# Performance work log

Hardware: AMD Instinct MI355X
Metric: run time of the kernel (lower is better)

## Reference

```python
import jax, jax.numpy as jnp
import numpy as np


def setup_inputs() -> dict:
    key = jax.random.key(0)
    k1, k2 = jax.random.split(key)
    enc_output = jax.random.normal(k1, (4, 4096, 1024), dtype=jnp.float32)
    dec_output = jax.random.normal(k2, (4, 4096, 1024), dtype=jnp.float32)
    return {"enc_output": enc_output, "dec_output": dec_output}


def reference(enc_output, dec_output):
    # a_t[b, e, t] = sum_d enc[b, e, d] * dec[b, t, d]   -> [B, T_enc, T_dec]
    a_t = jnp.einsum('bed,btd->bet', enc_output, dec_output)
    # softmax over dim=1 (the T_enc axis), no scaling, no mask (faithful to source)
    a_t = jax.nn.softmax(a_t, axis=1)
    # c_t[b, t, d] = sum_e a_t[b, e, t] * enc[b, e, d]   -> [B, T_dec, D]
    c_t = jnp.einsum('bet,bed->btd', a_t, enc_output)
    return c_t
```

## Files before the change

kernel.cpp:

```cpp
#include <hip/hip_runtime.h>
#include <hip/hip_fp16.h>

typedef _Float16 half_t;
typedef _Float16 f16x8 __attribute__((ext_vector_type(8)));
typedef _Float16 f16x4 __attribute__((ext_vector_type(4)));
typedef float f32x4 __attribute__((ext_vector_type(4)));

#define SEQ 4096
#define DDIM 1024
#define NBATCH 4

__device__ __forceinline__ void gload16(const half_t* g, half_t* l) {
  __builtin_amdgcn_global_load_lds((const __attribute__((address_space(1))) void*)g,
                                   (__attribute__((address_space(3))) void*)l, 16, 0, 0);
}

__global__ __launch_bounds__(256) void conv_f16(const float* __restrict__ src,
                                                half_t* __restrict__ dst) {
  int i = blockIdx.x * 256 + threadIdx.x;
  float4 x = ((const float4*)src)[i];
  f16x4 o = {(half_t)x.x, (half_t)x.y, (half_t)x.z, (half_t)x.w};
  *(f16x4*)(dst + (size_t)i * 4) = o;
}

__global__ __launch_bounds__(256) void transpose_f16(const float* __restrict__ src,
                                                     half_t* __restrict__ dst) {
  __shared__ float tile[32][33];
  int b = blockIdx.z;
  int e0 = blockIdx.x * 32, d0 = blockIdx.y * 32;
  const float* s = src + (size_t)b * SEQ * DDIM;
  half_t* dt = dst + (size_t)b * DDIM * SEQ;
  int tx = threadIdx.x & 31, ty = threadIdx.x >> 5;
#pragma unroll
  for (int i = 0; i < 4; i++) {
    int e = e0 + ty + i * 8;
    tile[ty + i * 8][tx] = s[(size_t)e * DDIM + d0 + tx];
  }
  __syncthreads();
#pragma unroll
  for (int i = 0; i < 4; i++) {
    int d = d0 + ty + i * 8;
    dt[(size_t)d * SEQ + e0 + tx] = (half_t)tile[tx][ty + i * 8];
  }
}

#define BM 128
#define BN 128
#define BK 64

__global__ __launch_bounds__(256) void gemm_f16(const half_t* __restrict__ A,
                                                const half_t* __restrict__ B,
                                                float* __restrict__ C, int M, int N, int K) {
  __shared__ __align__(16) half_t As[BM * BK];
  __shared__ __align__(16) half_t Bs[BN * BK];
  const int tid = threadIdx.x;
  const int bm = blockIdx.x, bn = blockIdx.y;
  const int wave = tid >> 6, lane = tid & 63;
  const int wm = (wave & 1) * 64, wn = (wave >> 1) * 64;
  const int mrow = lane & 15, quad = lane >> 4;

  f32x4 acc[4][4];
#pragma unroll
  for (int i = 0; i < 4; i++)
#pragma unroll
    for (int j = 0; j < 4; j++) acc[i][j] = {0.f, 0.f, 0.f, 0.f};

  const half_t* Ag = A + (size_t)(bm * BM) * K;
  const half_t* Bg = B + (size_t)(bn * BN) * K;

  for (int k0 = 0; k0 < K; k0 += BK) {
#pragma unroll
    for (int i = 0; i < 4; i++) {
      int cid = i * 256 + tid;
      int row = cid >> 3, slot = cid & 7;
      int chunk = slot ^ (row & 7);
      gload16(Ag + (size_t)row * K + k0 + chunk * 8, &As[row * BK + slot * 8]);
      gload16(Bg + (size_t)row * K + k0 + chunk * 8, &Bs[row * BK + slot * 8]);
    }
    __builtin_amdgcn_s_waitcnt(0);
    __syncthreads();
#pragma unroll
    for (int ks = 0; ks < 2; ks++) {
      f16x8 af[4], bf[4];
#pragma unroll
      for (int i = 0; i < 4; i++) {
        int ra = wm + i * 16 + mrow;
        int rb = wn + i * 16 + mrow;
        int sa = (ks * 4 + quad) ^ (ra & 7);
        int sb = (ks * 4 + quad) ^ (rb & 7);
        af[i] = *(const f16x8*)(&As[ra * BK + sa * 8]);
        bf[i] = *(const f16x8*)(&Bs[rb * BK + sb * 8]);
      }
#pragma unroll
      for (int mi = 0; mi < 4; mi++)
#pragma unroll
        for (int ni = 0; ni < 4; ni++)
          acc[mi][ni] =
              __builtin_amdgcn_mfma_f32_16x16x32_f16(af[mi], bf[ni], acc[mi][ni], 0, 0, 0);
    }
    __syncthreads();
  }
#pragma unroll
  for (int mi = 0; mi < 4; mi++) {
#pragma unroll
    for (int ni = 0; ni < 4; ni++) {
      int row0 = bm * BM + wm + mi * 16 + quad * 4;
      int col = bn * BN + wn + ni * 16 + mrow;
      float* Cp = C + (size_t)row0 * N + col;
#pragma unroll
      for (int r = 0; r < 4; r++) Cp[(size_t)r * N] = acc[mi][ni][r];
    }
  }
}

__global__ __launch_bounds__(256) void softmax_rows(const float* __restrict__ S,
                                                    half_t* __restrict__ P) {
  const int row = blockIdx.x;
  const float4* Sr = (const float4*)(S + (size_t)row * SEQ);
  const int tid = threadIdx.x, lane = tid & 63, wave = tid >> 6;
  __shared__ float red[4];
  __shared__ float bc;
  float4 v[4];
  float m = -1e30f;
#pragma unroll
  for (int j = 0; j < 4; j++) {
    v[j] = Sr[tid + j * 256];
    m = fmaxf(m, fmaxf(fmaxf(v[j].x, v[j].y), fmaxf(v[j].z, v[j].w)));
  }
#pragma unroll
  for (int o = 32; o; o >>= 1) m = fmaxf(m, __shfl_xor(m, o));
  if (lane == 0) red[wave] = m;
  __syncthreads();
  if (tid == 0) bc = fmaxf(fmaxf(red[0], red[1]), fmaxf(red[2], red[3]));
  __syncthreads();
  m = bc;
  float s = 0.f;
#pragma unroll
  for (int j = 0; j < 4; j++) {
    v[j].x = __expf(v[j].x - m);
    v[j].y = __expf(v[j].y - m);
    v[j].z = __expf(v[j].z - m);
    v[j].w = __expf(v[j].w - m);
    s += v[j].x + v[j].y + v[j].z + v[j].w;
  }
#pragma unroll
  for (int o = 32; o; o >>= 1) s += __shfl_xor(s, o);
  __syncthreads();
  if (lane == 0) red[wave] = s;
  __syncthreads();
  if (tid == 0) bc = red[0] + red[1] + red[2] + red[3];
  __syncthreads();
  float r = 1.0f / bc;
  f16x4* Pr = (f16x4*)(P + (size_t)row * SEQ);
#pragma unroll
  for (int j = 0; j < 4; j++) {
    f16x4 o = {(half_t)(v[j].x * r), (half_t)(v[j].y * r), (half_t)(v[j].z * r),
               (half_t)(v[j].w * r)};
    Pr[tid + j * 256] = o;
  }
}

__global__ __launch_bounds__(256) void naive_attn(const float* __restrict__ enc,
                                                  const float* __restrict__ dec,
                                                  float* __restrict__ out) {
  const int b = blockIdx.y, t = blockIdx.x;
  const float* encb = enc + (size_t)b * SEQ * DDIM;
  const float* q = dec + ((size_t)b * SEQ + t) * DDIM;
  __shared__ float qs[DDIM];
  __shared__ float sc[SEQ];
  __shared__ float red[4];
  __shared__ float bc;
  const int tid = threadIdx.x, lane = tid & 63, wave = tid >> 6;
  for (int i = tid; i < DDIM; i += 256) qs[i] = q[i];
  __syncthreads();
  for (int e = tid; e < SEQ; e += 256) {
    const float* er = encb + (size_t)e * DDIM;
    float s = 0.f;
    for (int d = 0; d < DDIM; d += 4) {
      float4 ev = *(const float4*)(er + d);
      s += ev.x * qs[d] + ev.y * qs[d + 1] + ev.z * qs[d + 2] + ev.w * qs[d + 3];
    }
    sc[e] = s;
  }
  __syncthreads();
  float m = -1e30f;
  for (int e = tid; e < SEQ; e += 256) m = fmaxf(m, sc[e]);
#pragma unroll
  for (int o = 32; o; o >>= 1) m = fmaxf(m, __shfl_xor(m, o));
  if (lane == 0) red[wave] = m;
  __syncthreads();
  if (tid == 0) bc = fmaxf(fmaxf(red[0], red[1]), fmaxf(red[2], red[3]));
  __syncthreads();
  m = bc;
  float s = 0.f;
  for (int e = tid; e < SEQ; e += 256) {
    float p = __expf(sc[e] - m);
    sc[e] = p;
    s += p;
  }
#pragma unroll
  for (int o = 32; o; o >>= 1) s += __shfl_xor(s, o);
  __syncthreads();
  if (lane == 0) red[wave] = s;
  __syncthreads();
  if (tid == 0) bc = red[0] + red[1] + red[2] + red[3];
  __syncthreads();
  const float rinv = 1.0f / bc;
  const int d0 = tid * 4;
  float4 acc = {0.f, 0.f, 0.f, 0.f};
  for (int e = 0; e < SEQ; e++) {
    float p = sc[e];
    float4 ev = *(const float4*)(encb + (size_t)e * DDIM + d0);
    acc.x += p * ev.x;
    acc.y += p * ev.y;
    acc.z += p * ev.z;
    acc.w += p * ev.w;
  }
  float4* o4 = (float4*)(out + ((size_t)b * SEQ + t) * DDIM + d0);
  float4 res = {acc.x * rinv, acc.y * rinv, acc.z * rinv, acc.w * rinv};
  *o4 = res;
}

extern "C" void kernel_launch(void* const* d_in, const int* in_sizes, int n_in, void* d_out,
                              int out_size, void* d_ws, size_t ws_size, hipStream_t stream) {
  const float* enc = (const float*)d_in[0];
  const float* dec = (const float*)d_in[1];
  float* out = (float*)d_out;

  const size_t SZ_S = (size_t)SEQ * SEQ * 4;
  const size_t SZ_P = (size_t)SEQ * SEQ * 2;
  const size_t SZ_H = (size_t)NBATCH * SEQ * DDIM * 2;
  const size_t NEED = SZ_S + SZ_P + 3 * SZ_H;

  if (ws_size >= NEED) {
    char* w = (char*)d_ws;
    float* S = (float*)w;
    half_t* P = (half_t*)(w + SZ_S);
    half_t* decF = (half_t*)(w + SZ_S + SZ_P);
    half_t* encF = (half_t*)(w + SZ_S + SZ_P + SZ_H);
    half_t* encT = (half_t*)(w + SZ_S + SZ_P + 2 * SZ_H);

    const int nconv = NBATCH * SEQ * DDIM / 4 / 256;
    conv_f16<<<nconv, 256, 0, stream>>>(dec, decF);
    conv_f16<<<nconv, 256, 0, stream>>>(enc, encF);
    transpose_f16<<<dim3(SEQ / 32, DDIM / 32, NBATCH), 256, 0, stream>>>(enc, encT);

    for (int b = 0; b < NBATCH; b++) {
      const size_t eo = (size_t)b * SEQ * DDIM;
      gemm_f16<<<dim3(SEQ / BM, SEQ / BN), 256, 0, stream>>>(decF + eo, encF + eo, S, SEQ, SEQ,
                                                             DDIM);
      softmax_rows<<<SEQ, 256, 0, stream>>>(S, P);
      gemm_f16<<<dim3(SEQ / BM, DDIM / BN), 256, 0, stream>>>(P, encT + eo, out + eo, SEQ, DDIM,
                                                              SEQ);
    }
  } else {
    naive_attn<<<dim3(SEQ, NBATCH), 256, 0, stream>>>(enc, dec, out);
  }
}
```

Baseline: 773.1 us.

## Batch GEMM and softmax launches across batch and add grouped tile ordering

The per-batch loop of GEMM, softmax, GEMM is replaced by single launches that index the batch through blockIdx.z and per-batch strides, when the workspace can hold every batch's score and probability matrices. The 2D tile grid is linearized and swizzled into groups of eight M-tiles, so blocks that run together share B tiles in L2. This targets launch overhead and low CU occupancy in the second GEMM, which has only 256 blocks per batch. In exchange, the fast path needs a much larger workspace, and tiered fallbacks cover smaller workspaces.

```diff
diff --git a/kernel.cpp b/kernel.cpp
--- a/kernel.cpp
+++ b/kernel.cpp
@@ -47,14 +47,21 @@
 #define BM 128
 #define BN 128
 #define BK 64
+#define GM 8
 
 __global__ __launch_bounds__(256) void gemm_f16(const half_t* __restrict__ A,
                                                 const half_t* __restrict__ B,
-                                                float* __restrict__ C, int M, int N, int K) {
+                                                float* __restrict__ C, int M, int N, int K,
+                                                size_t sA, size_t sB, size_t sC) {
   __shared__ __align__(16) half_t As[BM * BK];
   __shared__ __align__(16) half_t Bs[BN * BK];
   const int tid = threadIdx.x;
-  const int bm = blockIdx.x, bn = blockIdx.y;
+  const int nbn = N / BN;
+  const int lin = blockIdx.x;
+  const int per_group = GM * nbn;
+  const int g = lin / per_group, r = lin % per_group;
+  const int bm = g * GM + (r % GM);
+  const int bn = r / GM;
   const int wave = tid >> 6, lane = tid & 63;
   const int wm = (wave & 1) * 64, wn = (wave >> 1) * 64;
   const int mrow = lane & 15, quad = lane >> 4;
@@ -65,8 +72,8 @@
 #pragma unroll
     for (int j = 0; j < 4; j++) acc[i][j] = {0.f, 0.f, 0.f, 0.f};
 
-  const half_t* Ag = A + (size_t)(bm * BM) * K;
-  const half_t* Bg = B + (size_t)(bn * BN) * K;
+  const half_t* Ag = A + (size_t)blockIdx.z * sA + (size_t)(bm * BM) * K;
+  const half_t* Bg = B + (size_t)blockIdx.z * sB + (size_t)(bn * BN) * K;
 
   for (int k0 = 0; k0 < K; k0 += BK) {
 #pragma unroll
@@ -100,23 +107,24 @@
     }
     __syncthreads();
   }
+  float* Cb = C + (size_t)blockIdx.z * sC;
 #pragma unroll
   for (int mi = 0; mi < 4; mi++) {
 #pragma unroll
     for (int ni = 0; ni < 4; ni++) {
       int row0 = bm * BM + wm + mi * 16 + quad * 4;
       int col = bn * BN + wn + ni * 16 + mrow;
-      float* Cp = C + (size_t)row0 * N + col;
-#pragma unroll
-      for (int r = 0; r < 4; r++) Cp[(size_t)r * N] = acc[mi][ni][r];
+      float* Cp = Cb + (size_t)row0 * N + col;
+#pragma unroll
+      for (int r2 = 0; r2 < 4; r2++) Cp[(size_t)r2 * N] = acc[mi][ni][r2];
     }
   }
 }
 
 __global__ __launch_bounds__(256) void softmax_rows(const float* __restrict__ S,
                                                     half_t* __restrict__ P) {
-  const int row = blockIdx.x;
-  const float4* Sr = (const float4*)(S + (size_t)row * SEQ);
+  const size_t rbase = ((size_t)blockIdx.y * SEQ + blockIdx.x) * SEQ;
+  const float4* Sr = (const float4*)(S + rbase);
   const int tid = threadIdx.x, lane = tid & 63, wave = tid >> 6;
   __shared__ float red[4];
   __shared__ float bc;
@@ -151,7 +159,7 @@
   if (tid == 0) bc = red[0] + red[1] + red[2] + red[3];
   __syncthreads();
   float r = 1.0f / bc;
-  f16x4* Pr = (f16x4*)(P + (size_t)row * SEQ);
+  f16x4* Pr = (f16x4*)(P + rbase);
 #pragma unroll
   for (int j = 0; j < 4; j++) {
     f16x4 o = {(half_t)(v[j].x * r), (half_t)(v[j].y * r), (half_t)(v[j].z * r),
@@ -227,31 +235,58 @@
   const float* dec = (const float*)d_in[1];
   float* out = (float*)d_out;
 
-  const size_t SZ_S = (size_t)SEQ * SEQ * 4;
-  const size_t SZ_P = (size_t)SEQ * SEQ * 2;
-  const size_t SZ_H = (size_t)NBATCH * SEQ * DDIM * 2;
-  const size_t NEED = SZ_S + SZ_P + 3 * SZ_H;
-
-  if (ws_size >= NEED) {
+  const size_t EL = (size_t)SEQ * DDIM;
+  const size_t SM = (size_t)SEQ * SEQ;
+  const size_t SZ_S1 = SM * 4;
+  const size_t SZ_SA = NBATCH * SZ_S1;
+  const size_t SZ_P1 = SM * 2;
+  const size_t SZ_PA = NBATCH * SZ_P1;
+  const size_t SZ_H = NBATCH * EL * 2;
+  const size_t NEED_A = SZ_SA + SZ_PA + 3 * SZ_H;
+  const size_t NEED_B = SZ_S1 + SZ_PA + 3 * SZ_H;
+  const size_t NEED_C = SZ_S1 + SZ_P1 + 3 * SZ_H;
+
+  const int GB1 = (SEQ / BM) * (SEQ / BN);
+  const int GB2 = (SEQ / BM) * (DDIM / BN);
+
+  if (ws_size >= NEED_C) {
+    int tier = (ws_size >= NEED_A) ? 0 : (ws_size >= NEED_B) ? 1 : 2;
+    const size_t s_sz = (tier == 0) ? SZ_SA : SZ_S1;
+    const size_t p_sz = (tier <= 1) ? SZ_PA : SZ_P1;
     char* w = (char*)d_ws;
     float* S = (float*)w;
-    half_t* P = (half_t*)(w + SZ_S);
-    half_t* decF = (half_t*)(w + SZ_S + SZ_P);
-    half_t* encF = (half_t*)(w + SZ_S + SZ_P + SZ_H);
-    half_t* encT = (half_t*)(w + SZ_S + SZ_P + 2 * SZ_H);
-
-    const int nconv = NBATCH * SEQ * DDIM / 4 / 256;
+    half_t* P = (half_t*)(w + s_sz);
+    half_t* decF = (half_t*)(w + s_sz + p_sz);
+    half_t* encF = (half_t*)(w + s_sz + p_sz + SZ_H);
+    half_t* encT = (half_t*)(w + s_sz + p_sz + 2 * SZ_H);
+
+    const int nconv = (int)(NBATCH * EL / 4 / 256);
     conv_f16<<<nconv, 256, 0, stream>>>(dec, decF);
     conv_f16<<<nconv, 256, 0, stream>>>(enc, encF);
     transpose_f16<<<dim3(SEQ / 32, DDIM / 32, NBATCH), 256, 0, stream>>>(enc, encT);
 
-    for (int b = 0; b < NBATCH; b++) {
-      const size_t eo = (size_t)b * SEQ * DDIM;
-      gemm_f16<<<dim3(SEQ / BM, SEQ / BN), 256, 0, stream>>>(decF + eo, encF + eo, S, SEQ, SEQ,
-                                                             DDIM);
-      softmax_rows<<<SEQ, 256, 0, stream>>>(S, P);
-      gemm_f16<<<dim3(SEQ / BM, DDIM / BN), 256, 0, stream>>>(P, encT + eo, out + eo, SEQ, DDIM,
-                                                              SEQ);
+    if (tier == 0) {
+      gemm_f16<<<dim3(GB1, 1, NBATCH), 256, 0, stream>>>(decF, encF, S, SEQ, SEQ, DDIM, EL, EL,
+                                                         SM);
+      softmax_rows<<<dim3(SEQ, NBATCH), 256, 0, stream>>>(S, P);
+      gemm_f16<<<dim3(GB2, 1, NBATCH), 256, 0, stream>>>(P, encT, out, SEQ, DDIM, SEQ, SM, EL,
+                                                         EL);
+    } else if (tier == 1) {
+      for (int b = 0; b < NBATCH; b++) {
+        gemm_f16<<<dim3(GB1, 1, 1), 256, 0, stream>>>(decF + b * EL, encF + b * EL, S, SEQ, SEQ,
+                                                      DDIM, 0, 0, 0);
+        softmax_rows<<<dim3(SEQ, 1), 256, 0, stream>>>(S, P + b * SM);
+      }
+      gemm_f16<<<dim3(GB2, 1, NBATCH), 256, 0, stream>>>(P, encT, out, SEQ, DDIM, SEQ, SM, EL,
+                                                         EL);
+    } else {
+      for (int b = 0; b < NBATCH; b++) {
+        gemm_f16<<<dim3(GB1, 1, 1), 256, 0, stream>>>(decF + b * EL, encF + b * EL, S, SEQ, SEQ,
+                                                      DDIM, 0, 0, 0);
+        softmax_rows<<<dim3(SEQ, 1), 256, 0, stream>>>(S, P);
+        gemm_f16<<<dim3(GB2, 1, 1), 256, 0, stream>>>(P, encT + b * EL, out + b * EL, SEQ, DDIM,
+                                                      SEQ, 0, 0, 0);
+      }
     }
   } else {
     naive_attn<<<dim3(SEQ, NBATCH), 256, 0, stream>>>(enc, dec, out);
```

Result: slower. 793.8 us (+2.7%).
